# Kernel optimization log

Measured on AMD Instinct MI355X. Metric: run time of the kernel, lower is better.

## Reference

```python
import jax, jax.numpy as jnp
import numpy as np

N_EMBD = 1024
N_HEAD = 16
HEAD_SIZE = N_EMBD // N_HEAD  # 64
HEAD_INDEX = 0
# ALiBi slope: x = (2**8)**(1/n_head); slope = 1 / x**(head_index+1)
SLOPE = 1.0 / ((2.0 ** 8) ** (1.0 / N_HEAD)) ** (HEAD_INDEX + 1)
B, T = 4, 4096


def setup_inputs() -> dict:
    key = jax.random.key(0)
    kx, kq, kk, kv = jax.random.split(key, 4)
    x = jax.random.normal(kx, (B, T, N_EMBD), dtype=jnp.float32)
    wq = jax.random.normal(kq, (HEAD_SIZE, N_EMBD), dtype=jnp.float32) * 0.02
    wk = jax.random.normal(kk, (HEAD_SIZE, N_EMBD), dtype=jnp.float32) * 0.02
    wv = jax.random.normal(kv, (HEAD_SIZE, N_EMBD), dtype=jnp.float32) * 0.02
    return {"x": x, "wq": wq, "wk": wk, "wv": wv}


def reference(x, wq, wk, wv):
    Bq, Tq, C = x.shape
    q = jnp.einsum('btc,hc->bth', x, wq)  # [B,T,Hd]
    k = jnp.einsum('btc,hc->bth', x, wk)
    v = jnp.einsum('btc,hc->bth', x, wv)
    # NOTE: original scales by C**-0.5 where C = n_embd (full dim), not head_size
    wei = jnp.einsum('bth,bsh->bts', q, k) * (C ** -0.5)  # [B,T,T]
    idx = jnp.arange(Tq)
    distance = idx[None, :] - idx[:, None]  # [T,T], j - i
    wei = wei + distance.astype(wei.dtype) * jnp.asarray(SLOPE, wei.dtype)
    causal = distance <= 0  # tril: key index j <= query index i
    wei = jnp.where(causal[None, :, :], wei, -jnp.inf)
    wei = jax.nn.softmax(wei, axis=-1)
    out = jnp.einsum('bts,bsh->bth', wei, v)  # [B,T,Hd]
    return out
```

## Files before the change

### kernel.cpp

```cpp
#include <hip/hip_runtime.h>
#include <hip/hip_bf16.h>
#include <stdint.h>
#include <math.h>

typedef __attribute__((ext_vector_type(8))) short bf16x8;
typedef __attribute__((ext_vector_type(4))) float f32x4;

#define TSEQ 4096
#define LOG2E 1.44269504088896340736f
#define SLOPE 0.70710678118654752440f
#define SL2E (SLOPE * LOG2E)

__device__ __forceinline__ unsigned short f32_to_bf16(float f) {
  union { float f; unsigned int u; } v; v.f = f;
  unsigned int r = v.u + 0x7fffu + ((v.u >> 16) & 1u);
  return (unsigned short)(r >> 16);
}

__device__ __forceinline__ unsigned int pk2(float a, float b) {
  union { __hip_bfloat162 h; unsigned int u; } c;
  c.h = __float22bfloat162_rn(make_float2(a, b));
  return c.u;
}
__device__ __forceinline__ bf16x8 cvt8(f32x4 a, f32x4 b) {
  union { unsigned int u[4]; bf16x8 v; } r;
  r.u[0] = pk2(a[0], a[1]); r.u[1] = pk2(a[2], a[3]);
  r.u[2] = pk2(b[0], b[1]); r.u[3] = pk2(b[2], b[3]);
  return r.v;
}

__device__ __forceinline__ void async_cp16(const void* g, void* l) {
  __builtin_amdgcn_global_load_lds(
      (const __attribute__((address_space(1))) unsigned int*)g,
      (__attribute__((address_space(3))) unsigned int*)l, 16, 0, 0);
}

__global__ __launch_bounds__(256) void init_kernel(
    const float* __restrict__ wq, const float* __restrict__ wk,
    const float* __restrict__ wv, unsigned short* __restrict__ Wb,
    unsigned short* __restrict__ vt) {
  int tid = blockIdx.x * 256 + threadIdx.x;
  if (tid < 24576) {
    int lane = tid & 63, s = (tid >> 6) & 31, nt = (tid >> 11) & 3, t = tid >> 13;
    int n = nt * 16 + (lane & 15);
    int k = s * 32 + (lane >> 4) * 8;
    const float* src = (t == 0 ? wq : (t == 1 ? wk : wv)) + (size_t)n * 1024 + k;
    f32x4 a = *(const f32x4*)src;
    f32x4 b = *(const f32x4*)(src + 4);
    if (t == 0) {
#pragma unroll
      for (int j = 0; j < 4; ++j) { a[j] *= 0.03125f; b[j] *= 0.03125f; }
    }
    *(bf16x8*)(Wb + (size_t)tid * 8) = cvt8(a, b);
  }
  int b2 = tid >> 15, off = (tid & 32767) * 2;
  *(unsigned int*)(vt + (size_t)b2 * 327680 + 262144 + off) = 0x3F803F80u;
}

__global__ __launch_bounds__(256, 2) void proj_kernel(
    const float* __restrict__ x, const unsigned short* __restrict__ Wb,
    unsigned short* __restrict__ qb, unsigned short* __restrict__ kb,
    unsigned short* __restrict__ vt) {
  __shared__ float xbuf[32][64];
  __shared__ unsigned short wbuf[12][2][64][8];

  const int lane = threadIdx.x & 63;
  const int wave = threadIdx.x >> 6;
  const int l16 = lane & 15, quad = lane >> 4;
  const int R0 = blockIdx.x * 32;
  const int ci0 = wave * 3;

  f32x4 acc[2][3];
#pragma unroll
  for (int st = 0; st < 2; ++st)
#pragma unroll
    for (int j = 0; j < 3; ++j) acc[st][j] = (f32x4){0.f, 0.f, 0.f, 0.f};

  const int rA = wave * 8 + quad;
  const int rB = rA + 4;
  const int gA = l16 ^ (rA & 15);
  const int gB = l16 ^ (rB & 15);
  const float* srcA = x + (size_t)(R0 + rA) * 1024 + gA * 4;
  const float* srcB = x + (size_t)(R0 + rB) * 1024 + gB * 4;
  float* dstA = &xbuf[wave * 8][0];
  float* dstB = &xbuf[wave * 8 + 4][0];

  for (int step = 0; step < 16; ++step) {
    const int k0 = step * 64;
    async_cp16(srcA + k0, dstA);
    async_cp16(srcB + k0, dstB);
#pragma unroll
    for (int j = 0; j < 3; ++j) {
      const unsigned short* wsrc = Wb + ((size_t)((ci0 + j) * 32 + step * 2) * 64 + lane) * 8;
      async_cp16(wsrc, &wbuf[ci0 + j][0][0][0]);
      async_cp16(wsrc + 512, &wbuf[ci0 + j][1][0][0]);
    }
    __syncthreads();

#pragma unroll
    for (int ss = 0; ss < 2; ++ss) {
      bf16x8 af[2];
#pragma unroll
      for (int st = 0; st < 2; ++st) {
        const float* base = &xbuf[st * 16 + l16][0];
        f32x4 a0 = *(const f32x4*)(base + ((ss * 8 + quad * 2) ^ l16) * 4);
        f32x4 a1 = *(const f32x4*)(base + ((ss * 8 + quad * 2 + 1) ^ l16) * 4);
        af[st] = cvt8(a0, a1);
      }
#pragma unroll
      for (int j = 0; j < 3; ++j) {
        bf16x8 wfr = *(const bf16x8*)&wbuf[ci0 + j][ss][lane][0];
        acc[0][j] = __builtin_amdgcn_mfma_f32_16x16x32_bf16(af[0], wfr, acc[0][j], 0, 0, 0);
        acc[1][j] = __builtin_amdgcn_mfma_f32_16x16x32_bf16(af[1], wfr, acc[1][j], 0, 0, 0);
      }
    }
    __syncthreads();
  }

#pragma unroll
  for (int st = 0; st < 2; ++st) {
#pragma unroll
    for (int j = 0; j < 3; ++j) {
      const int ci = ci0 + j;
#pragma unroll
      for (int r = 0; r < 4; ++r) {
        int row = R0 + st * 16 + quad * 4 + r;
        unsigned short hv = f32_to_bf16(acc[st][j][r]);
        if (ci < 4) {
          qb[(size_t)row * 64 + ci * 16 + l16] = hv;
        } else if (ci < 8) {
          kb[(size_t)row * 64 + (ci - 4) * 16 + l16] = hv;
        } else {
          int b = row >> 12, tt = row & 4095;
          vt[((size_t)b * 80 + (ci - 8) * 16 + l16) * TSEQ + tt] = hv;
        }
      }
    }
  }
}

__global__ __launch_bounds__(256, 4) void attn_kernel(
    const unsigned short* __restrict__ qb, const unsigned short* __restrict__ kb,
    const unsigned short* __restrict__ vt, float* __restrict__ out) {
  __shared__ unsigned short pbuf[4][16][40];
  __shared__ float obuf[4][5][16][17];

  const int lane = threadIdx.x & 63;
  const int wave = threadIdx.x >> 6;
  const int l16 = lane & 15, quad = lane >> 4;
  const int tid = blockIdx.x;
  const int b = tid & 3;
  const int r0 = (tid >> 2) << 4;
  const int j0 = (r0 > 112) ? (r0 - 112) : 0;
  const int jb = j0 + wave * 32;

  const unsigned short* kbase = kb + (size_t)b * TSEQ * 64;
  const unsigned short* vbase = vt + (size_t)b * 80 * TSEQ;

  const unsigned short* qrow = qb + (size_t)(b * TSEQ + r0 + l16) * 64 + quad * 8;
  bf16x8 qa0 = *(const bf16x8*)qrow;
  bf16x8 qa1 = *(const bf16x8*)(qrow + 32);

  f32x4 o[5];
#pragma unroll
  for (int dt = 0; dt < 5; ++dt) o[dt] = (f32x4){0.f, 0.f, 0.f, 0.f};

  const int irel = jb + l16 - r0 - quad * 4;
  const float fb = SL2E * (float)irel;

#pragma unroll
  for (int nt = 0; nt < 2; ++nt) {
    const unsigned short* krow = kbase + (size_t)(jb + nt * 16 + l16) * 64 + quad * 8;
    f32x4 sa = (f32x4){0.f, 0.f, 0.f, 0.f};
    sa = __builtin_amdgcn_mfma_f32_16x16x32_bf16(qa0, *(const bf16x8*)krow, sa, 0, 0, 0);
    sa = __builtin_amdgcn_mfma_f32_16x16x32_bf16(qa1, *(const bf16x8*)(krow + 32), sa, 0, 0, 0);
#pragma unroll
    for (int r = 0; r < 4; ++r) {
      float arg = fmaf(sa[r], LOG2E, fb + SL2E * (float)(nt * 16 - r));
      float p = exp2f(arg);
      if (irel + nt * 16 - r > 0) p = 0.f;
      pbuf[wave][quad * 4 + r][nt * 16 + l16] = f32_to_bf16(p);
    }
  }
  bf16x8 pa = *(const bf16x8*)&pbuf[wave][l16][quad * 8];

#pragma unroll
  for (int dt = 0; dt < 5; ++dt) {
    const unsigned short* vrow = vbase + (size_t)(dt * 16 + l16) * TSEQ + jb + quad * 8;
    o[dt] = __builtin_amdgcn_mfma_f32_16x16x32_bf16(pa, *(const bf16x8*)vrow, o[dt], 0, 0, 0);
  }

#pragma unroll
  for (int dt = 0; dt < 5; ++dt)
#pragma unroll
    for (int r = 0; r < 4; ++r)
      obuf[wave][dt][quad * 4 + r][l16] = o[dt][r];

  __syncthreads();

  const int rr = threadIdx.x >> 4;
  const int c0 = (threadIdx.x & 15) * 4;
  const int dt = c0 >> 4, cc = c0 & 15;
  float l = obuf[0][4][rr][0] + obuf[1][4][rr][0] + obuf[2][4][rr][0] + obuf[3][4][rr][0];
  float invl = 1.0f / l;
  f32x4 res;
#pragma unroll
  for (int i = 0; i < 4; ++i)
    res[i] = (obuf[0][dt][rr][cc + i] + obuf[1][dt][rr][cc + i] +
              obuf[2][dt][rr][cc + i] + obuf[3][dt][rr][cc + i]) * invl;
  *(f32x4*)(out + (size_t)(b * TSEQ + r0 + rr) * 64 + c0) = res;
}

extern "C" void kernel_launch(void* const* d_in, const int* in_sizes, int n_in,
                              void* d_out, int out_size, void* d_ws, size_t ws_size,
                              hipStream_t stream) {
  const float* x  = (const float*)d_in[0];
  const float* wq = (const float*)d_in[1];
  const float* wk = (const float*)d_in[2];
  const float* wv = (const float*)d_in[3];
  float* out = (float*)d_out;

  char* ws = (char*)d_ws;
  unsigned short* Wb = (unsigned short*)(ws);
  unsigned short* qb = (unsigned short*)(ws + 393216);
  unsigned short* kb = (unsigned short*)(ws + 393216 + 2097152);
  unsigned short* vt = (unsigned short*)(ws + 393216 + 2 * 2097152);

  init_kernel<<<512, 256, 0, stream>>>(wq, wk, wv, Wb, vt);
  proj_kernel<<<512, 256, 0, stream>>>(x, Wb, qb, kb, vt);
  attn_kernel<<<1024, 256, 0, stream>>>(qb, kb, vt, out);
}
```

Baseline: 124.4 us.

## Load x directly into registers in projection, drop x LDS staging

The projection kernel now loads the fp32 x tile straight from global memory into registers in the MFMA fragment layout, instead of staging it through a swizzled LDS buffer. The K-step is doubled to 128, so there are half as many barrier iterations, and the weight LDS buffer grows to four slices. Occupancy is raised to three blocks per SM. This removes LDS round trips and barriers for x, but adds register pressure and uncoalesced 32-byte-strided global reads.

```diff
diff --git a/kernel.cpp b/kernel.cpp
--- a/kernel.cpp
+++ b/kernel.cpp
@@ -57,12 +57,11 @@
   *(unsigned int*)(vt + (size_t)b2 * 327680 + 262144 + off) = 0x3F803F80u;
 }
 
-__global__ __launch_bounds__(256, 2) void proj_kernel(
+__global__ __launch_bounds__(256, 3) void proj_kernel(
     const float* __restrict__ x, const unsigned short* __restrict__ Wb,
     unsigned short* __restrict__ qb, unsigned short* __restrict__ kb,
     unsigned short* __restrict__ vt) {
-  __shared__ float xbuf[32][64];
-  __shared__ unsigned short wbuf[12][2][64][8];
+  __shared__ unsigned short wbuf[12][4][64][8];
 
   const int lane = threadIdx.x & 63;
   const int wave = threadIdx.x >> 6;
@@ -76,42 +75,38 @@
 #pragma unroll
     for (int j = 0; j < 3; ++j) acc[st][j] = (f32x4){0.f, 0.f, 0.f, 0.f};
 
-  const int rA = wave * 8 + quad;
-  const int rB = rA + 4;
-  const int gA = l16 ^ (rA & 15);
-  const int gB = l16 ^ (rB & 15);
-  const float* srcA = x + (size_t)(R0 + rA) * 1024 + gA * 4;
-  const float* srcB = x + (size_t)(R0 + rB) * 1024 + gB * 4;
-  float* dstA = &xbuf[wave * 8][0];
-  float* dstB = &xbuf[wave * 8 + 4][0];
-
-  for (int step = 0; step < 16; ++step) {
-    const int k0 = step * 64;
-    async_cp16(srcA + k0, dstA);
-    async_cp16(srcB + k0, dstB);
-#pragma unroll
-    for (int j = 0; j < 3; ++j) {
-      const unsigned short* wsrc = Wb + ((size_t)((ci0 + j) * 32 + step * 2) * 64 + lane) * 8;
-      async_cp16(wsrc, &wbuf[ci0 + j][0][0][0]);
-      async_cp16(wsrc + 512, &wbuf[ci0 + j][1][0][0]);
-    }
+  const float* xb0 = x + (size_t)(R0 + l16) * 1024 + quad * 8;
+  const float* xb1 = xb0 + 16 * 1024;
+  const unsigned short* wsrc0 = Wb + ((size_t)(ci0 * 32) * 64 + lane) * 8;
+
+#pragma unroll 1
+  for (int step = 0; step < 8; ++step) {
+    f32x4 xr[2][4][2];
+#pragma unroll
+    for (int ss = 0; ss < 4; ++ss) {
+#pragma unroll
+      for (int p = 0; p < 2; ++p) {
+        xr[0][ss][p] = *(const f32x4*)(xb0 + step * 128 + ss * 32 + p * 4);
+        xr[1][ss][p] = *(const f32x4*)(xb1 + step * 128 + ss * 32 + p * 4);
+      }
+    }
+#pragma unroll
+    for (int j = 0; j < 3; ++j)
+#pragma unroll
+      for (int ss = 0; ss < 4; ++ss)
+        async_cp16(wsrc0 + ((size_t)(j * 32 + step * 4 + ss) * 64) * 8,
+                   &wbuf[ci0 + j][ss][0][0]);
     __syncthreads();
 
 #pragma unroll
-    for (int ss = 0; ss < 2; ++ss) {
-      bf16x8 af[2];
-#pragma unroll
-      for (int st = 0; st < 2; ++st) {
-        const float* base = &xbuf[st * 16 + l16][0];
-        f32x4 a0 = *(const f32x4*)(base + ((ss * 8 + quad * 2) ^ l16) * 4);
-        f32x4 a1 = *(const f32x4*)(base + ((ss * 8 + quad * 2 + 1) ^ l16) * 4);
-        af[st] = cvt8(a0, a1);
-      }
+    for (int ss = 0; ss < 4; ++ss) {
+      bf16x8 af0 = cvt8(xr[0][ss][0], xr[0][ss][1]);
+      bf16x8 af1 = cvt8(xr[1][ss][0], xr[1][ss][1]);
 #pragma unroll
       for (int j = 0; j < 3; ++j) {
         bf16x8 wfr = *(const bf16x8*)&wbuf[ci0 + j][ss][lane][0];
-        acc[0][j] = __builtin_amdgcn_mfma_f32_16x16x32_bf16(af[0], wfr, acc[0][j], 0, 0, 0);
-        acc[1][j] = __builtin_amdgcn_mfma_f32_16x16x32_bf16(af[1], wfr, acc[1][j], 0, 0, 0);
+        acc[0][j] = __builtin_amdgcn_mfma_f32_16x16x32_bf16(af0, wfr, acc[0][j], 0, 0, 0);
+        acc[1][j] = __builtin_amdgcn_mfma_f32_16x16x32_bf16(af1, wfr, acc[1][j], 0, 0, 0);
       }
     }
     __syncthreads();
```

Measured after the change: 138.3 us. +11.2%, slower.
